# Kernel optimization log

Hardware: AMD Instinct MI355X
Metric: run time of the kernel (lower is better)

## Reference

```python
import jax, jax.numpy as jnp
import numpy as np

B, L, CH, NH, NB = 32, 512, 512, 8, 2
HD = CH // NH
NEG = -4294967295.0  # -2**32 + 1, as in the torch code


def _ln(x, g, b, eps=1e-8):
    m = x.mean(-1, keepdims=True)
    v = ((x - m) ** 2).mean(-1, keepdims=True)
    return (x - m) / jnp.sqrt(v + eps) * g + b


def _forward(log_seqs, seqs_nxt, t, qw, qb, kw, kb, vw, vb,
             ln1g, ln1b, ln2g, ln2b, c1w, c1b, c2w, c2b,
             posK, posV, lng, lnb, tw0, tb0, tw1, tb1, tw2, tb2,
             decw, decb):
    # causal mask (mode='training'): True = masked (~tril)
    mask = jnp.triu(jnp.ones((L, L), dtype=bool), k=1)
    pK = posK[:L].reshape(L, NH, HD)  # shared relative/absolute pos per head
    pV = posV[:L].reshape(L, NH, HD)
    seqs = log_seqs
    for i in range(NB):
        Qin = _ln(seqs, ln1g[i], ln1b[i])
        # note: Q from layernormed input, K/V from raw seqs (as in torch code)
        Q = (Qin @ qw[i].T + qb[i]).reshape(B, L, NH, HD)
        K = (seqs @ kw[i].T + kb[i]).reshape(B, L, NH, HD)
        V = (seqs @ vw[i].T + vb[i]).reshape(B, L, NH, HD)
        scores = jnp.einsum('blhd,bmhd->bhlm', Q, K)
        scores = scores + jnp.einsum('blhd,mhd->bhlm', Q, pK)
        scores = scores / jnp.sqrt(jnp.float32(HD))
        scores = jnp.where(mask, NEG, scores)
        w = jax.nn.softmax(scores, axis=-1)
        out = jnp.einsum('bhlm,bmhd->blhd', w, V) + jnp.einsum('bhlm,mhd->blhd', w, pV)
        seqs = Qin + out.reshape(B, L, CH)  # residual from layernormed Q
        seqs = _ln(seqs, ln2g[i], ln2b[i])
        # PointWiseFeedForward: conv1d kernel_size=1 == linear; residual inside
        h = jax.nn.relu(seqs @ c1w[i].T + c1b[i])
        seqs = seqs + (h @ c2w[i].T + c2b[i])
    log_feats = _ln(seqs, lng, lnb)

    # diffusion timestep embedding
    half = CH // 2
    freqs = jnp.exp(jnp.arange(half, dtype=jnp.float32) * (-np.log(10000.0) / (half - 1)))
    ang = t.astype(jnp.float32)[:, None] * freqs[None, :]
    temb = jnp.concatenate([jnp.sin(ang), jnp.cos(ang)], axis=1)  # [B, CH]
    temb = temb @ tw0.T + tb0
    temb = temb * jax.nn.sigmoid(temb)  # swish nonlinearity
    temb = temb @ tw1.T + tb1
    temb = temb * jax.nn.sigmoid(temb)
    temb = temb @ tw2.T + tb2
    x_t = seqs_nxt + temb[:, None, :]

    # non-conditional decoder path: decoder(cat([log_feats, x_t], -1))
    dec = jnp.concatenate([log_feats, x_t], axis=-1) @ decw.T + decb
    return (log_feats, dec)


def setup_inputs() -> dict:
    key = jax.random.key(0)
    ks = jax.random.split(key, 24)
    s = 0.02

    def n(k, shape):
        return jax.random.normal(k, shape, jnp.float32) * s

    return {
        'log_seqs': jax.random.normal(ks[0], (B, L, CH), jnp.float32),
        'seqs_nxt': jax.random.normal(ks[1], (B, L, CH), jnp.float32),
        't': jax.random.randint(ks[2], (B,), 0, 1000, jnp.int32),
        'qw': n(ks[3], (NB, CH, CH)), 'qb': jnp.zeros((NB, CH), jnp.float32),
        'kw': n(ks[4], (NB, CH, CH)), 'kb': jnp.zeros((NB, CH), jnp.float32),
        'vw': n(ks[5], (NB, CH, CH)), 'vb': jnp.zeros((NB, CH), jnp.float32),
        'ln1g': jnp.ones((NB, CH), jnp.float32), 'ln1b': jnp.zeros((NB, CH), jnp.float32),
        'ln2g': jnp.ones((NB, CH), jnp.float32), 'ln2b': jnp.zeros((NB, CH), jnp.float32),
        'c1w': n(ks[6], (NB, CH, CH)), 'c1b': jnp.zeros((NB, CH), jnp.float32),
        'c2w': n(ks[7], (NB, CH, CH)), 'c2b': jnp.zeros((NB, CH), jnp.float32),
        'posK': n(ks[8], (L, CH)), 'posV': n(ks[9], (L, CH)),
        'lng': jnp.ones((CH,), jnp.float32), 'lnb': jnp.zeros((CH,), jnp.float32),
        'tw0': n(ks[10], (4 * CH, CH)), 'tb0': jnp.zeros((4 * CH,), jnp.float32),
        'tw1': n(ks[11], (4 * CH, 4 * CH)), 'tb1': jnp.zeros((4 * CH,), jnp.float32),
        'tw2': n(ks[12], (CH, 4 * CH)), 'tb2': jnp.zeros((CH,), jnp.float32),
        'decw': n(ks[13], (CH, 2 * CH)), 'decb': jnp.zeros((CH,), jnp.float32),
    }


def reference(log_seqs, seqs_nxt, t, qw, qb, kw, kb, vw, vb,
              ln1g, ln1b, ln2g, ln2b, c1w, c1b, c2w, c2b,
              posK, posV, lng, lnb, tw0, tb0, tw1, tb1, tw2, tb2,
              decw, decb):
    return _forward(log_seqs, seqs_nxt, t, qw, qb, kw, kb, vw, vb,
                    ln1g, ln1b, ln2g, ln2b, c1w, c1b, c2w, c2b,
                    posK, posV, lng, lnb, tw0, tb0, tw1, tb1, tw2, tb2,
                    decw, decb)
```

## Files before the change

kernel.cpp:

```cpp
#include <hip/hip_runtime.h>
#include <math.h>

#define BB 32
#define LL 512
#define CHN 512
#define NHH 8
#define HDD 64

typedef __attribute__((ext_vector_type(8))) short short8;
typedef __attribute__((ext_vector_type(4))) float f32x4;

__device__ __forceinline__ float b2f(unsigned short s) {
    union { unsigned int u; float f; } c; c.u = ((unsigned int)s) << 16; return c.f;
}
__device__ __forceinline__ unsigned short f2b(float f) {
    union { float f; unsigned int u; } c; c.f = f;
    return (unsigned short)((c.u + 0x7fffu + ((c.u >> 16) & 1u)) >> 16);
}

#define SWZ(row, col) ((((row) * 64 + (col))) ^ (((row) & 7) << 3))

__device__ __forceinline__ void gl16(const unsigned short* g, unsigned short* l) {
    __builtin_amdgcn_global_load_lds(
        (const __attribute__((address_space(1))) unsigned int*)g,
        (__attribute__((address_space(3))) unsigned int*)l, 16, 0, 0);
}

__global__ __launch_bounds__(256) void cvt7_kernel(
    const float* __restrict__ p0, const float* __restrict__ p1,
    const float* __restrict__ p2, const float* __restrict__ p3,
    const float* __restrict__ p4, const float* __restrict__ p5,
    unsigned short* __restrict__ y,
    const float* __restrict__ seqs, unsigned short* __restrict__ R1)
{
    const int j = blockIdx.y;
    const int i = blockIdx.x * 256 + threadIdx.x;
    if (j < 6) {
        const float* x = j == 0 ? p0 : j == 1 ? p1 : j == 2 ? p2
                       : j == 3 ? p3 : j == 4 ? p4 : p5;
        const float4 v = reinterpret_cast<const float4*>(x)[i];
        ushort4 o;
        o.x = f2b(v.x); o.y = f2b(v.y); o.z = f2b(v.z); o.w = f2b(v.w);
        size_t dst4;
        if (j == 1)      dst4 = 131072 + i + (i >= 65536 ? 65536 : 0);
        else if (j == 2) dst4 = 131072 + 65536 + i + (i >= 65536 ? 65536 : 0);
        else             dst4 = (size_t)j * 131072 + i;
        reinterpret_cast<ushort4*>(y)[dst4] = o;
    } else {
        #pragma unroll
        for (int t = 0; t < 16; ++t) {
            const int ii = t * 131072 + i;
            const float4 v = reinterpret_cast<const float4*>(seqs)[ii];
            ushort4 o;
            o.x = f2b(v.x); o.y = f2b(v.y); o.z = f2b(v.z); o.w = f2b(v.w);
            reinterpret_cast<ushort4*>(R1)[ii] = o;
        }
    }
}

__global__ __launch_bounds__(256) void ln_kernel(
    const unsigned short* __restrict__ x, const float* __restrict__ g,
    const float* __restrict__ b, float* __restrict__ yf,
    unsigned short* __restrict__ yb)
{
    const int row = blockIdx.x;
    const int tid = threadIdx.x;
    const size_t base = (size_t)row * CHN;
    const ushort2 v2 = *reinterpret_cast<const ushort2*>(x + base + tid * 2);
    const float vx = b2f(v2.x), vy = b2f(v2.y);
    float s  = vx + vy;
    float ss = vx * vx + vy * vy;
    #pragma unroll
    for (int m = 1; m < 64; m <<= 1) {
        s  += __shfl_xor(s, m);
        ss += __shfl_xor(ss, m);
    }
    __shared__ float red[8];
    const int wave = tid >> 6;
    if ((tid & 63) == 0) { red[wave] = s; red[4 + wave] = ss; }
    __syncthreads();
    s  = red[0] + red[1] + red[2] + red[3];
    ss = red[4] + red[5] + red[6] + red[7];
    const float mean = s * (1.0f / CHN);
    const float var  = ss * (1.0f / CHN) - mean * mean;
    const float inv  = rsqrtf(var + 1e-8f);
    const int c = tid * 2;
    float ox = (vx - mean) * inv * g[c]     + b[c];
    float oy = (vy - mean) * inv * g[c + 1] + b[c + 1];
    if (yf) *reinterpret_cast<float2*>(yf + base + c) = make_float2(ox, oy);
    if (yb) {
        ushort2 ob; ob.x = f2b(ox); ob.y = f2b(oy);
        *reinterpret_cast<ushort2*>(yb + base + c) = ob;
    }
}

template <int NT, int NBX>
__device__ __forceinline__ void gemm_body(
    const unsigned short* __restrict__ A,
    const unsigned short* __restrict__ A2,
    const unsigned short* __restrict__ W, int ldw,
    const float* __restrict__ bias,
    const float* __restrict__ pos,
    const unsigned short* __restrict__ resb,
    float* __restrict__ outf,
    unsigned short* __restrict__ outb,
    unsigned short* __restrict__ outbt,
    int act, int bid,
    unsigned short* lA, unsigned short* lB)
{
    const int tid  = threadIdx.x;
    const int lane = tid & 63;
    const int wid  = tid >> 6;

    const int swz = (bid & 7) * (NBX * 8) + (bid >> 3);
    const int by = swz / NBX, bx = swz % NBX;
    const int bm = by * 256, bn = bx * 128;

    const int ia0 = wid * 2, ia1 = wid * 2 + 1;
    const int hiA0 = ia0 >> 2, rgA0 = ia0 & 3;
    const int hiA1 = ia1 >> 2, rgA1 = ia1 & 3;
    const int hiB = wid >> 1, rgB = wid & 1;

    const unsigned short* Ax = A2 ? A2 : A;
    const unsigned short* aS0  = A  + (size_t)(bm + rgA0 * 64 + lane) * 512 + hiA0 * 8;
    const unsigned short* aS1  = A  + (size_t)(bm + rgA1 * 64 + lane) * 512 + hiA1 * 8;
    const unsigned short* a2S0 = Ax + (size_t)(bm + rgA0 * 64 + lane) * 512 + hiA0 * 8;
    const unsigned short* a2S1 = Ax + (size_t)(bm + rgA1 * 64 + lane) * 512 + hiA1 * 8;
    const unsigned short* wS   = W + (size_t)(bn + rgB * 64 + lane) * ldw + hiB * 8;
    const int dA0 = (hiA0 * 256 + rgA0 * 64) * 8;
    const int dA1 = (hiA1 * 256 + rgA1 * 64) * 8;
    const int dB  = (hiB * 128 + rgB * 64) * 8;

    const int wr = wid >> 1, wc = wid & 1;
    const int fr = lane & 15;
    const int fq = lane >> 4;

    f32x4 acc[4][4];
    #pragma unroll
    for (int m = 0; m < 4; ++m)
        #pragma unroll
        for (int n = 0; n < 4; ++n)
            acc[m][n] = (f32x4){0.f, 0.f, 0.f, 0.f};

    #define MG_STAGE(buf, t)                                            \
        do {                                                            \
            const int k0 = ((t) & 15) * 32;                             \
            const unsigned short* s0 = ((t) < 16) ? aS0 : a2S0;         \
            const unsigned short* s1 = ((t) < 16) ? aS1 : a2S1;         \
            gl16(s0 + k0, &lA[(buf) * 8192 + dA0]);                     \
            gl16(s1 + k0, &lA[(buf) * 8192 + dA1]);                     \
            gl16(wS + (t) * 32, &lB[(buf) * 4096 + dB]);                \
        } while (0)

    MG_STAGE(0, 0);
    MG_STAGE(1, 1);

    #pragma unroll
    for (int t = 0; t < NT; ++t) {
        const int cur = t % 3;
        if (t + 2 < NT) {
            MG_STAGE((t + 2) % 3, t + 2);
            asm volatile("s_waitcnt vmcnt(6)" ::: "memory");
        } else if (t + 1 < NT) {
            asm volatile("s_waitcnt vmcnt(3)" ::: "memory");
        } else {
            asm volatile("s_waitcnt vmcnt(0)" ::: "memory");
        }
        __builtin_amdgcn_s_barrier();

        const unsigned short* pa = &lA[cur * 8192 + (fq * 256 + wr * 64 + fr) * 8];
        const unsigned short* pb = &lB[cur * 4096 + (fq * 128 + wc * 64 + fr) * 8];
        short8 aF[4], bF[4];
        #pragma unroll
        for (int m = 0; m < 4; ++m)
            aF[m] = *reinterpret_cast<const short8*>(pa + m * 128);
        #pragma unroll
        for (int n = 0; n < 4; ++n)
            bF[n] = *reinterpret_cast<const short8*>(pb + n * 128);
        asm volatile("s_waitcnt lgkmcnt(0)" ::: "memory");
        __builtin_amdgcn_s_barrier();

        __builtin_amdgcn_s_setprio(1);
        #pragma unroll
        for (int m = 0; m < 4; ++m)
            #pragma unroll
            for (int n = 0; n < 4; ++n)
                acc[m][n] = __builtin_amdgcn_mfma_f32_16x16x32_bf16(
                    aF[m], bF[n], acc[m][n], 0, 0, 0);
        __builtin_amdgcn_s_setprio(0);
    }
    #undef MG_STAGE

    const int row0 = bm + wr * 64, col0 = bn + wc * 64;
    #pragma unroll
    for (int m = 0; m < 4; ++m) {
        #pragma unroll
        for (int n = 0; n < 4; ++n) {
            const int col = col0 + n * 16 + fr;
            const float bia = bias ? bias[col] : 0.f;
            ushort4 o4;
            #pragma unroll
            for (int r = 0; r < 4; ++r) {
                const int row = row0 + m * 16 + fq * 4 + r;
                float v = acc[m][n][r] + bia;
                if (pos) v += pos[(size_t)(row & (LL - 1)) * CHN + col];
                if (act == 1) v = fmaxf(v, 0.f);
                else if (act == 3) v *= 0.125f;
                const size_t idx = (size_t)row * CHN + col;
                if (resb) v += b2f(resb[idx]);
                if (outf) outf[idx] = v;
                if (outb) outb[idx] = f2b(v);
                ((unsigned short*)&o4)[r] = f2b(v);
            }
            if (outbt) {
                const int rw = row0 + m * 16 + fq * 4;
                *reinterpret_cast<ushort4*>(
                    &outbt[((size_t)(rw >> 9) * 512 + col) * 512 + (rw & 511)]) = o4;
            }
        }
    }
}

__device__ __forceinline__ void kv_body(
    const unsigned short* __restrict__ A,
    const unsigned short* __restrict__ Wkv,
    const float* __restrict__ kb, const float* __restrict__ vb,
    const float* __restrict__ posK, const float* __restrict__ posV,
    unsigned short* __restrict__ KBb, unsigned short* __restrict__ VTb,
    int bid, unsigned short* lA, unsigned short* lB)
{
    const int tid  = threadIdx.x;
    const int lane = tid & 63;
    const int wid  = tid >> 6;

    const int swz = (bid & 7) * 64 + (bid >> 3);
    const int by = swz >> 3, bx = swz & 7;
    const int bm = by * 256, bn = bx * 128;

    const int ia0 = wid * 2, ia1 = wid * 2 + 1;
    const int hiA0 = ia0 >> 2, rgA0 = ia0 & 3;
    const int hiA1 = ia1 >> 2, rgA1 = ia1 & 3;
    const int hiB = wid >> 1, rgB = wid & 1;

    const unsigned short* aS0 = A + (size_t)(bm + rgA0 * 64 + lane) * 512 + hiA0 * 8;
    const unsigned short* aS1 = A + (size_t)(bm + rgA1 * 64 + lane) * 512 + hiA1 * 8;
    const unsigned short* wS  = Wkv + (size_t)(bn + rgB * 64 + lane) * 512 + hiB * 8;
    const int dA0 = (hiA0 * 256 + rgA0 * 64) * 8;
    const int dA1 = (hiA1 * 256 + rgA1 * 64) * 8;
    const int dB  = (hiB * 128 + rgB * 64) * 8;

    const int wr = wid >> 1, wc = wid & 1;
    const int fr = lane & 15;
    const int fq = lane >> 4;

    f32x4 acc[4][4];
    #pragma unroll
    for (int m = 0; m < 4; ++m)
        #pragma unroll
        for (int n = 0; n < 4; ++n)
            acc[m][n] = (f32x4){0.f, 0.f, 0.f, 0.f};

    #define KV_STAGE(buf, t)                                            \
        do {                                                            \
            const int k0 = (t) * 32;                                    \
            gl16(aS0 + k0, &lA[(buf) * 8192 + dA0]);                    \
            gl16(aS1 + k0, &lA[(buf) * 8192 + dA1]);                    \
            gl16(wS + k0, &lB[(buf) * 4096 + dB]);                      \
        } while (0)

    KV_STAGE(0, 0);
    KV_STAGE(1, 1);

    #pragma unroll
    for (int t = 0; t < 16; ++t) {
        const int cur = t % 3;
        if (t + 2 < 16) {
            KV_STAGE((t + 2) % 3, t + 2);
            asm volatile("s_waitcnt vmcnt(6)" ::: "memory");
        } else if (t + 1 < 16) {
            asm volatile("s_waitcnt vmcnt(3)" ::: "memory");
        } else {
            asm volatile("s_waitcnt vmcnt(0)" ::: "memory");
        }
        __builtin_amdgcn_s_barrier();

        const unsigned short* pa = &lA[cur * 8192 + (fq * 256 + wr * 64 + fr) * 8];
        const unsigned short* pb = &lB[cur * 4096 + (fq * 128 + wc * 64 + fr) * 8];
        short8 aF[4], bF[4];
        #pragma unroll
        for (int m = 0; m < 4; ++m)
            aF[m] = *reinterpret_cast<const short8*>(pa + m * 128);
        #pragma unroll
        for (int n = 0; n < 4; ++n)
            bF[n] = *reinterpret_cast<const short8*>(pb + n * 128);
        asm volatile("s_waitcnt lgkmcnt(0)" ::: "memory");
        __builtin_amdgcn_s_barrier();

        __builtin_amdgcn_s_setprio(1);
        #pragma unroll
        for (int m = 0; m < 4; ++m)
            #pragma unroll
            for (int n = 0; n < 4; ++n)
                acc[m][n] = __builtin_amdgcn_mfma_f32_16x16x32_bf16(
                    aF[m], bF[n], acc[m][n], 0, 0, 0);
        __builtin_amdgcn_s_setprio(0);
    }
    #undef KV_STAGE

    const int row0 = bm + wr * 64;
    if (bn < 512) {
        const int col0 = bn + wc * 64;
        #pragma unroll
        for (int m = 0; m < 4; ++m) {
            #pragma unroll
            for (int n = 0; n < 4; ++n) {
                const int col = col0 + n * 16 + fr;
                const float bia = kb[col];
                #pragma unroll
                for (int r = 0; r < 4; ++r) {
                    const int row = row0 + m * 16 + fq * 4 + r;
                    float v = acc[m][n][r] + bia
                            + posK[(size_t)(row & (LL - 1)) * CHN + col];
                    KBb[(size_t)row * CHN + col] = f2b(v);
                }
            }
        }
    } else {
        const int vcol0 = (bn - 512) + wc * 64;
        #pragma unroll
        for (int m = 0; m < 4; ++m) {
            #pragma unroll
            for (int n = 0; n < 4; ++n) {
                const int vcol = vcol0 + n * 16 + fr;
                const float bia = vb[vcol];
                ushort4 o4;
                #pragma unroll
                for (int r = 0; r < 4; ++r) {
                    const int row = row0 + m * 16 + fq * 4 + r;
                    float v = acc[m][n][r] + bia
                            + posV[(size_t)(row & (LL - 1)) * CHN + vcol];
                    ((unsigned short*)&o4)[r] = f2b(v);
                }
                const int rw = row0 + m * 16 + fq * 4;
                *reinterpret_cast<ushort4*>(
                    &VTb[((size_t)(rw >> 9) * 512 + vcol) * 512 + (rw & 511)]) = o4;
            }
        }
    }
}

__global__ __launch_bounds__(512) void mgemm_kernel(
    const unsigned short* __restrict__ A,
    const unsigned short* __restrict__ W, int ldw,
    const float* __restrict__ bias,
    const float* __restrict__ pos,
    const unsigned short* __restrict__ resb,
    float* __restrict__ outf,
    unsigned short* __restrict__ outb,
    unsigned short* __restrict__ outbt,
    int act)
{
    __shared__ alignas(16) unsigned short lA[3 * 8192];
    __shared__ alignas(16) unsigned short lB[3 * 4096];
    gemm_body<16, 4>(A, nullptr, W, ldw, bias, pos, resb, outf, outb, outbt, act,
                     blockIdx.x, lA, lB);
}

__global__ __launch_bounds__(512) void qkv2_kernel(
    const unsigned short* __restrict__ qinb, const unsigned short* __restrict__ curb,
    const unsigned short* __restrict__ Wq, const unsigned short* __restrict__ Wkv,
    const float* __restrict__ qb, const float* __restrict__ kb,
    const float* __restrict__ vb,
    const float* __restrict__ posK, const float* __restrict__ posV,
    unsigned short* __restrict__ QBb, unsigned short* __restrict__ KBb,
    unsigned short* __restrict__ VTb)
{
    __shared__ alignas(16) unsigned short lA[3 * 8192];
    __shared__ alignas(16) unsigned short lB[3 * 4096];
    if (blockIdx.x < 256) {
        gemm_body<16, 4>(qinb, nullptr, Wq, 512, qb, nullptr, nullptr,
                         nullptr, QBb, nullptr, 3, blockIdx.x, lA, lB);
    } else {
        kv_body(curb, Wkv, kb, vb, posK, posV, KBb, VTb, blockIdx.x - 256, lA, lB);
    }
}

__global__ __launch_bounds__(512) void dec_kernel(
    const unsigned short* __restrict__ R0b, const unsigned short* __restrict__ R1b,
    const unsigned short* __restrict__ Wd, const float* __restrict__ decb,
    float* __restrict__ dec)
{
    __shared__ alignas(16) unsigned short lA[3 * 8192];
    __shared__ alignas(16) unsigned short lB[3 * 4096];
    gemm_body<32, 4>(R0b, R1b, Wd, 1024, decb, nullptr, nullptr, dec, nullptr,
                     nullptr, 0, blockIdx.x, lA, lB);
}

__global__ __launch_bounds__(256) void skgemm_kernel(
    const float* __restrict__ A, int K,
    const float* __restrict__ W, int N,
    float* __restrict__ P)
{
    __shared__ float As[32][128];
    const int tid = threadIdx.x;
    const int kz  = blockIdx.y;
    const int c   = blockIdx.x * 256 + tid;

    #pragma unroll
    for (int i = 0; i < 16; ++i) {
        const int idx = i * 256 + tid;
        const int r = idx >> 7, k = idx & 127;
        As[r][k] = A[(size_t)r * K + kz * 128 + k];
    }
    __syncthreads();

    float acc[32];
    #pragma unroll
    for (int r = 0; r < 32; ++r) acc[r] = 0.f;

    const float* wrow = W + (size_t)c * K + kz * 128;
    for (int k4 = 0; k4 < 32; ++k4) {
        const float4 w = reinterpret_cast<const float4*>(wrow)[k4];
        #pragma unroll
        for (int r = 0; r < 32; ++r) {
            const float4 a = *reinterpret_cast<const float4*>(&As[r][k4 * 4]);
            acc[r] = fmaf(w.x, a.x, fmaf(w.y, a.y, fmaf(w.z, a.z, fmaf(w.w, a.w, acc[r]))));
        }
    }

    float* pp = P + ((size_t)kz * N + c) * 32;
    #pragma unroll
    for (int r = 0; r < 32; ++r) pp[r] = acc[r];
}

__global__ __launch_bounds__(256) void skreduce_kernel(
    const float* __restrict__ P, int KS, const float* __restrict__ bias,
    float* __restrict__ out, int N, int act)
{
    const int idx = blockIdx.x * 256 + threadIdx.x;
    const int r = idx & 31, c = idx >> 5;
    float s = 0.f;
    for (int kz = 0; kz < KS; ++kz)
        s += P[(size_t)kz * N * 32 + idx];
    s += bias[c];
    if (act == 2) s = s / (1.f + __expf(-s));
    out[(size_t)r * N + c] = s;
}

__global__ __launch_bounds__(256) void mattn_kernel(
    const unsigned short* __restrict__ Q, const unsigned short* __restrict__ K,
    const unsigned short* __restrict__ VT, const unsigned short* __restrict__ Qin,
    unsigned short* __restrict__ Sout)
{
    __shared__ alignas(16) unsigned short kT[2][4096];
    __shared__ alignas(16) unsigned short vT[2][4096];
    __shared__ unsigned short pl[4][1024];

    const int pr = blockIdx.x;
    const int qtA = pr, qtB = 7 - pr;
    const int h  = blockIdx.y;
    const int b  = blockIdx.z;
    const int tid = threadIdx.x, lane = tid & 63, wid = tid >> 6;
    const int fr = lane & 15, fq = lane >> 4;
    const int hc = h * HDD;

    const int c0i = tid, c1i = 256 + tid;
    const int r0s = c0i >> 3, j0s = c0i & 7, d0s = ((j0s ^ (r0s & 7)) << 3);
    const int r1s = c1i >> 3, j1s = c1i & 7, d1s = ((j1s ^ (r1s & 7)) << 3);
    const unsigned short* kS0 = K + (size_t)b * LL * CHN + (size_t)r0s * CHN + hc + d0s;
    const unsigned short* kS1 = K + (size_t)b * LL * CHN + (size_t)r1s * CHN + hc + d1s;
    const unsigned short* vS0 = VT + ((size_t)(b * NHH + h) * 64 + r0s) * 512 + d0s;
    const unsigned short* vS1 = VT + ((size_t)(b * NHH + h) * 64 + r1s) * 512 + d1s;

    #define AT_STAGE(buf, ch)                                              \
        do {                                                               \
            const int o = (ch) * 64;                                       \
            gl16(kS0 + (size_t)o * CHN, &kT[buf][wid * 512]);              \
            gl16(kS1 + (size_t)o * CHN, &kT[buf][2048 + wid * 512]);       \
            gl16(vS0 + o, &vT[buf][wid * 512]);                            \
            gl16(vS1 + o, &vT[buf][2048 + wid * 512]);                     \
        } while (0)

    const size_t qrowA = (size_t)b * LL + qtA * 64 + wid * 16 + fr;
    const size_t qrowB = (size_t)b * LL + qtB * 64 + wid * 16 + fr;
    short8 qfA[2], qfB[2];
    qfA[0] = *reinterpret_cast<const short8*>(Q + qrowA * CHN + hc + fq * 8);
    qfA[1] = *reinterpret_cast<const short8*>(Q + qrowA * CHN + hc + 32 + fq * 8);
    qfB[0] = *reinterpret_cast<const short8*>(Q + qrowB * CHN + hc + fq * 8);
    qfB[1] = *reinterpret_cast<const short8*>(Q + qrowB * CHN + hc + 32 + fq * 8);

    f32x4 oaccA[4], oaccB[4];
    float lA_[4], lB_[4];
    #pragma unroll
    for (int n = 0; n < 4; ++n) {
        oaccA[n] = (f32x4){0.f, 0.f, 0.f, 0.f};
        oaccB[n] = (f32x4){0.f, 0.f, 0.f, 0.f};
    }
    #pragma unroll
    for (int r = 0; r < 4; ++r) { lA_[r] = 0.f; lB_[r] = 0.f; }

    auto tile_step = [&](int cur, int qt, int ch, const short8* qf,
                         f32x4* oacc, float* lrow) {
        f32x4 sacc[4];
        #pragma unroll
        for (int n = 0; n < 4; ++n) sacc[n] = (f32x4){0.f, 0.f, 0.f, 0.f};
        __builtin_amdgcn_s_setprio(1);
        #pragma unroll
        for (int kk = 0; kk < 2; ++kk) {
            #pragma unroll
            for (int n = 0; n < 4; ++n) {
                const short8 kf = *reinterpret_cast<const short8*>(
                    &kT[cur][SWZ(n * 16 + fr, kk * 32 + fq * 8)]);
                sacc[n] = __builtin_amdgcn_mfma_f32_16x16x32_bf16(qf[kk], kf, sacc[n], 0, 0, 0);
            }
        }
        __builtin_amdgcn_s_setprio(0);

        const bool diag = (ch == qt);
        #pragma unroll
        for (int r = 0; r < 4; ++r) {
            float sv[4];
            #pragma unroll
            for (int n = 0; n < 4; ++n) {
                float v = sacc[n][r];
                if (diag && (n * 16 + fr > wid * 16 + fq * 4 + r)) v = -1e30f;
                sv[n] = __expf(v);
            }
            float ps = (sv[0] + sv[1]) + (sv[2] + sv[3]);
            ps += __shfl_xor(ps, 1);
            ps += __shfl_xor(ps, 2);
            ps += __shfl_xor(ps, 4);
            ps += __shfl_xor(ps, 8);
            lrow[r] += ps;
            #pragma unroll
            for (int n = 0; n < 4; ++n)
                pl[wid][SWZ(fq * 4 + r, n * 16 + fr)] = f2b(sv[n]);
        }

        __builtin_amdgcn_s_setprio(1);
        #pragma unroll
        for (int kk = 0; kk < 2; ++kk) {
            const short8 pa = *reinterpret_cast<const short8*>(
                &pl[wid][SWZ(fr, kk * 32 + fq * 8)]);
            #pragma unroll
            for (int n = 0; n < 4; ++n) {
                const short8 vf = *reinterpret_cast<const short8*>(
                    &vT[cur][SWZ(n * 16 + fr, kk * 32 + fq * 8)]);
                oacc[n] = __builtin_amdgcn_mfma_f32_16x16x32_bf16(pa, vf, oacc[n], 0, 0, 0);
            }
        }
        __builtin_amdgcn_s_setprio(0);
    };

    AT_STAGE(0, 0);
    __syncthreads();

    for (int ch = 0; ch <= qtB; ++ch) {
        const int cur = ch & 1;
        if (ch < qtB) AT_STAGE(cur ^ 1, ch + 1);

        tile_step(cur, qtB, ch, qfB, oaccB, lB_);
        if (ch <= qtA)
            tile_step(cur, qtA, ch, qfA, oaccA, lA_);

        __syncthreads();
    }
    #undef AT_STAGE

    #pragma unroll
    for (int s = 0; s < 2; ++s) {
        const int qt = s ? qtB : qtA;
        const f32x4* oacc = s ? oaccB : oaccA;
        const float* lrow = s ? lB_ : lA_;
        const size_t orow0 = (size_t)b * LL + qt * 64 + wid * 16 + fq * 4;
        #pragma unroll
        for (int r = 0; r < 4; ++r) {
            const float inv = 1.f / lrow[r];
            const size_t rowidx = (orow0 + r) * CHN + hc;
            #pragma unroll
            for (int n = 0; n < 4; ++n) {
                const int d = n * 16 + fr;
                Sout[rowidx + d] = f2b(oacc[n][r] * inv + b2f(Qin[rowidx + d]));
            }
        }
    }
}

__global__ __launch_bounds__(256) void temb_embed_kernel(
    const int* __restrict__ t, float* __restrict__ T0)
{
    const int idx = blockIdx.x * 256 + threadIdx.x;
    const int b = idx >> 9, j = idx & 511;
    const float tv = (float)t[b];
    const int jj = (j < 256) ? j : j - 256;
    const float freq = __expf((float)jj * (-9.210340371976184f / 255.f));
    const float ang = tv * freq;
    T0[idx] = (j < 256) ? sinf(ang) : cosf(ang);
}

__global__ __launch_bounds__(256) void add_temb_kernel(
    const float* __restrict__ xin, const float* __restrict__ temb,
    unsigned short* __restrict__ out)
{
    const size_t i4 = (size_t)blockIdx.x * 256 + threadIdx.x;
    const size_t elem = i4 * 4;
    const int b = (int)(elem >> 18);
    const int c = (int)(elem & (CHN - 1));
    const float4 a = reinterpret_cast<const float4*>(xin)[i4];
    const float4 tv = *reinterpret_cast<const float4*>(temb + (size_t)b * CHN + c);
    ushort4 o;
    o.x = f2b(a.x + tv.x); o.y = f2b(a.y + tv.y);
    o.z = f2b(a.z + tv.z); o.w = f2b(a.w + tv.w);
    reinterpret_cast<ushort4*>(out)[i4] = o;
}

extern "C" void kernel_launch(void* const* d_in, const int* in_sizes, int n_in,
                              void* d_out, int out_size, void* d_ws, size_t ws_size,
                              hipStream_t stream)
{
    (void)in_sizes; (void)n_in; (void)out_size; (void)ws_size;
    const float* log_seqs = (const float*)d_in[0];
    const float* seqs_nxt = (const float*)d_in[1];
    const int*   tt       = (const int*)d_in[2];
    const float* qw  = (const float*)d_in[3];
    const float* qb  = (const float*)d_in[4];
    const float* kw  = (const float*)d_in[5];
    const float* kb  = (const float*)d_in[6];
    const float* vw  = (const float*)d_in[7];
    const float* vb  = (const float*)d_in[8];
    const float* ln1g = (const float*)d_in[9];
    const float* ln1b = (const float*)d_in[10];
    const float* ln2g = (const float*)d_in[11];
    const float* ln2b = (const float*)d_in[12];
    const float* c1w = (const float*)d_in[13];
    const float* c1b = (const float*)d_in[14];
    const float* c2w = (const float*)d_in[15];
    const float* c2b = (const float*)d_in[16];
    const float* posK = (const float*)d_in[17];
    const float* posV = (const float*)d_in[18];
    const float* lng = (const float*)d_in[19];
    const float* lnb = (const float*)d_in[20];
    const float* tw0 = (const float*)d_in[21];
    const float* tb0 = (const float*)d_in[22];
    const float* tw1 = (const float*)d_in[23];
    const float* tb1 = (const float*)d_in[24];
    const float* tw2 = (const float*)d_in[25];
    const float* tb2 = (const float*)d_in[26];
    const float* decw = (const float*)d_in[27];
    const float* decb = (const float*)d_in[28];

    const size_t SZ = (size_t)BB * LL * CHN;
    const int M = BB * LL;
    float* out = (float*)d_out;
    float* log_feats = out;
    float* dec = out + SZ;
    unsigned short* QBb = (unsigned short*)dec;
    unsigned short* VTb = (unsigned short*)log_feats;

    float* ws = (float*)d_ws;
    unsigned short* SB = (unsigned short*)ws;
    float* P = ws + SZ / 2;
    unsigned short* KBb = (unsigned short*)(ws + SZ);
    unsigned short* R0  = (unsigned short*)(ws + SZ + SZ / 2);
    unsigned short* R1  = (unsigned short*)(ws + 2 * SZ);
    unsigned short* WBu = (unsigned short*)(ws + 2 * SZ + SZ / 2);
    float* T0 = ws + 2 * SZ + SZ / 2 + 1572864;
    float* T1 = T0 + 32 * CHN;
    float* T2 = T1 + 32 * 2048;
    float* T3 = T2 + 32 * 2048;

    const size_t WQ = 0, WKV = 524288, WC1 = 1572864,
                 WC2 = 2097152, WDEC = 2621440;

    auto mg = [&](const unsigned short* A, const unsigned short* W, int ldw,
                  const float* bias, const float* pos, const unsigned short* resb,
                  float* outf, unsigned short* outb, unsigned short* outbt, int act) {
        mgemm_kernel<<<256, 512, 0, stream>>>(A, W, ldw, bias, pos, resb,
                                              outf, outb, outbt, act);
    };
    auto skg = [&](const float* A, int K, const float* W, int N,
                   const float* bias, float* o, int act) {
        skgemm_kernel<<<dim3(N / 256, K / 128), 256, 0, stream>>>(A, K, W, N, P);
        skreduce_kernel<<<(N * 32) / 256, 256, 0, stream>>>(P, K / 128, bias, o, N, act);
    };

    cvt7_kernel<<<dim3(512, 7), 256, 0, stream>>>(qw, kw, vw, c1w, c2w, decw, WBu,
                                                  log_seqs, R1);

    for (int i = 0; i < 2; ++i) {
        const size_t wo = (size_t)i * 262144;
        const size_t bo = (size_t)i * CHN;

        ln_kernel<<<M, 256, 0, stream>>>(R1, ln1g + bo, ln1b + bo, nullptr, R0);
        qkv2_kernel<<<768, 512, 0, stream>>>(
            R0, R1, WBu + WQ + wo, WBu + WKV + (size_t)i * 524288,
            qb + bo, kb + bo, vb + bo, posK, posV, QBb, KBb, VTb);
        mattn_kernel<<<dim3(4, NHH, BB), 256, 0, stream>>>(QBb, KBb, VTb, R0, SB);
        ln_kernel<<<M, 256, 0, stream>>>(SB, ln2g + bo, ln2b + bo, nullptr, SB);
        mg(SB, WBu + WC1 + wo, 512, c1b + bo, nullptr, nullptr, nullptr, R0, nullptr, 1);
        mg(R0, WBu + WC2 + wo, 512, c2b + bo, nullptr, SB, nullptr, R1, nullptr, 0);
    }

    ln_kernel<<<M, 256, 0, stream>>>(R1, lng, lnb, log_feats, R0);

    temb_embed_kernel<<<(BB * CHN) / 256, 256, 0, stream>>>(tt, T0);
    skg(T0, 512, tw0, 2048, tb0, T1, 2);
    skg(T1, 2048, tw1, 2048, tb1, T2, 2);
    skg(T2, 2048, tw2, 512, tb2, T3, 0);
    add_temb_kernel<<<(M * CHN / 4) / 256, 256, 0, stream>>>(seqs_nxt, T3, R1);

    dec_kernel<<<256, 512, 0, stream>>>(R0, R1, WBu + WDEC, decb, dec);
}
```

Before: 597.4 us.

## Split paired query tiles across two wave groups in 512-thread attention blocks

The attention kernel moves from 256 to 512 threads per block. Each group of four waves now handles one of the two paired query tiles, instead of every wave processing both tiles one after the other. This roughly halves the serial per-wave work and register state (one accumulator set), which should raise parallelism and occupancy. Each thread also issues half as many staging loads. In exchange, the qtA wave group goes idle for the chunks after its diagonal tile but still waits at every barrier, and LDS use grows for the larger P buffer.

```diff
diff --git a/kernel.cpp b/kernel.cpp
--- a/kernel.cpp
+++ b/kernel.cpp
@@ -447,110 +447,48 @@
     out[(size_t)r * N + c] = s;
 }
 
-__global__ __launch_bounds__(256) void mattn_kernel(
+__global__ __launch_bounds__(512) void mattn_kernel(
     const unsigned short* __restrict__ Q, const unsigned short* __restrict__ K,
     const unsigned short* __restrict__ VT, const unsigned short* __restrict__ Qin,
     unsigned short* __restrict__ Sout)
 {
     __shared__ alignas(16) unsigned short kT[2][4096];
     __shared__ alignas(16) unsigned short vT[2][4096];
-    __shared__ unsigned short pl[4][1024];
+    __shared__ unsigned short pl[8][1024];
 
     const int pr = blockIdx.x;
     const int qtA = pr, qtB = 7 - pr;
     const int h  = blockIdx.y;
     const int b  = blockIdx.z;
     const int tid = threadIdx.x, lane = tid & 63, wid = tid >> 6;
+    const int wg = wid >> 2;
+    const int wl = wid & 3;
     const int fr = lane & 15, fq = lane >> 4;
     const int hc = h * HDD;
 
-    const int c0i = tid, c1i = 256 + tid;
-    const int r0s = c0i >> 3, j0s = c0i & 7, d0s = ((j0s ^ (r0s & 7)) << 3);
-    const int r1s = c1i >> 3, j1s = c1i & 7, d1s = ((j1s ^ (r1s & 7)) << 3);
-    const unsigned short* kS0 = K + (size_t)b * LL * CHN + (size_t)r0s * CHN + hc + d0s;
-    const unsigned short* kS1 = K + (size_t)b * LL * CHN + (size_t)r1s * CHN + hc + d1s;
-    const unsigned short* vS0 = VT + ((size_t)(b * NHH + h) * 64 + r0s) * 512 + d0s;
-    const unsigned short* vS1 = VT + ((size_t)(b * NHH + h) * 64 + r1s) * 512 + d1s;
+    const int rs = tid >> 3, js = tid & 7, ds = ((js ^ (rs & 7)) << 3);
+    const unsigned short* kS = K + (size_t)b * LL * CHN + (size_t)rs * CHN + hc + ds;
+    const unsigned short* vS = VT + ((size_t)(b * NHH + h) * 64 + rs) * 512 + ds;
 
     #define AT_STAGE(buf, ch)                                              \
         do {                                                               \
             const int o = (ch) * 64;                                       \
-            gl16(kS0 + (size_t)o * CHN, &kT[buf][wid * 512]);              \
-            gl16(kS1 + (size_t)o * CHN, &kT[buf][2048 + wid * 512]);       \
-            gl16(vS0 + o, &vT[buf][wid * 512]);                            \
-            gl16(vS1 + o, &vT[buf][2048 + wid * 512]);                     \
+            gl16(kS + (size_t)o * CHN, &kT[buf][wid * 512]);               \
+            gl16(vS + o, &vT[buf][wid * 512]);                             \
         } while (0)
 
-    const size_t qrowA = (size_t)b * LL + qtA * 64 + wid * 16 + fr;
-    const size_t qrowB = (size_t)b * LL + qtB * 64 + wid * 16 + fr;
-    short8 qfA[2], qfB[2];
-    qfA[0] = *reinterpret_cast<const short8*>(Q + qrowA * CHN + hc + fq * 8);
-    qfA[1] = *reinterpret_cast<const short8*>(Q + qrowA * CHN + hc + 32 + fq * 8);
-    qfB[0] = *reinterpret_cast<const short8*>(Q + qrowB * CHN + hc + fq * 8);
-    qfB[1] = *reinterpret_cast<const short8*>(Q + qrowB * CHN + hc + 32 + fq * 8);
-
-    f32x4 oaccA[4], oaccB[4];
-    float lA_[4], lB_[4];
-    #pragma unroll
-    for (int n = 0; n < 4; ++n) {
-        oaccA[n] = (f32x4){0.f, 0.f, 0.f, 0.f};
-        oaccB[n] = (f32x4){0.f, 0.f, 0.f, 0.f};
-    }
-    #pragma unroll
-    for (int r = 0; r < 4; ++r) { lA_[r] = 0.f; lB_[r] = 0.f; }
-
-    auto tile_step = [&](int cur, int qt, int ch, const short8* qf,
-                         f32x4* oacc, float* lrow) {
-        f32x4 sacc[4];
-        #pragma unroll
-        for (int n = 0; n < 4; ++n) sacc[n] = (f32x4){0.f, 0.f, 0.f, 0.f};
-        __builtin_amdgcn_s_setprio(1);
-        #pragma unroll
-        for (int kk = 0; kk < 2; ++kk) {
-            #pragma unroll
-            for (int n = 0; n < 4; ++n) {
-                const short8 kf = *reinterpret_cast<const short8*>(
-                    &kT[cur][SWZ(n * 16 + fr, kk * 32 + fq * 8)]);
-                sacc[n] = __builtin_amdgcn_mfma_f32_16x16x32_bf16(qf[kk], kf, sacc[n], 0, 0, 0);
-            }
-        }
-        __builtin_amdgcn_s_setprio(0);
-
-        const bool diag = (ch == qt);
-        #pragma unroll
-        for (int r = 0; r < 4; ++r) {
-            float sv[4];
-            #pragma unroll
-            for (int n = 0; n < 4; ++n) {
-                float v = sacc[n][r];
-                if (diag && (n * 16 + fr > wid * 16 + fq * 4 + r)) v = -1e30f;
-                sv[n] = __expf(v);
-            }
-            float ps = (sv[0] + sv[1]) + (sv[2] + sv[3]);
-            ps += __shfl_xor(ps, 1);
-            ps += __shfl_xor(ps, 2);
-            ps += __shfl_xor(ps, 4);
-            ps += __shfl_xor(ps, 8);
-            lrow[r] += ps;
-            #pragma unroll
-            for (int n = 0; n < 4; ++n)
-                pl[wid][SWZ(fq * 4 + r, n * 16 + fr)] = f2b(sv[n]);
-        }
-
-        __builtin_amdgcn_s_setprio(1);
-        #pragma unroll
-        for (int kk = 0; kk < 2; ++kk) {
-            const short8 pa = *reinterpret_cast<const short8*>(
-                &pl[wid][SWZ(fr, kk * 32 + fq * 8)]);
-            #pragma unroll
-            for (int n = 0; n < 4; ++n) {
-                const short8 vf = *reinterpret_cast<const short8*>(
-                    &vT[cur][SWZ(n * 16 + fr, kk * 32 + fq * 8)]);
-                oacc[n] = __builtin_amdgcn_mfma_f32_16x16x32_bf16(pa, vf, oacc[n], 0, 0, 0);
-            }
-        }
-        __builtin_amdgcn_s_setprio(0);
-    };
+    const int myQt = wg ? qtA : qtB;
+    const size_t qrow = (size_t)b * LL + myQt * 64 + wl * 16 + fr;
+    short8 qf[2];
+    qf[0] = *reinterpret_cast<const short8*>(Q + qrow * CHN + hc + fq * 8);
+    qf[1] = *reinterpret_cast<const short8*>(Q + qrow * CHN + hc + 32 + fq * 8);
+
+    f32x4 oacc[4];
+    float lrow[4];
+    #pragma unroll
+    for (int n = 0; n < 4; ++n) oacc[n] = (f32x4){0.f, 0.f, 0.f, 0.f};
+    #pragma unroll
+    for (int r = 0; r < 4; ++r) lrow[r] = 0.f;
 
     AT_STAGE(0, 0);
     __syncthreads();
@@ -559,29 +497,73 @@
         const int cur = ch & 1;
         if (ch < qtB) AT_STAGE(cur ^ 1, ch + 1);
 
-        tile_step(cur, qtB, ch, qfB, oaccB, lB_);
-        if (ch <= qtA)
-            tile_step(cur, qtA, ch, qfA, oaccA, lA_);
+        if (ch <= myQt) {
+            f32x4 sacc[4];
+            #pragma unroll
+            for (int n = 0; n < 4; ++n) sacc[n] = (f32x4){0.f, 0.f, 0.f, 0.f};
+            __builtin_amdgcn_s_setprio(1);
+            #pragma unroll
+            for (int kk = 0; kk < 2; ++kk) {
+                #pragma unroll
+                for (int n = 0; n < 4; ++n) {
+                    const short8 kf = *reinterpret_cast<const short8*>(
+                        &kT[cur][SWZ(n * 16 + fr, kk * 32 + fq * 8)]);
+                    sacc[n] = __builtin_amdgcn_mfma_f32_16x16x32_bf16(
+                        qf[kk], kf, sacc[n], 0, 0, 0);
+                }
+            }
+            __builtin_amdgcn_s_setprio(0);
+
+            const bool diag = (ch == myQt);
+            #pragma unroll
+            for (int r = 0; r < 4; ++r) {
+                float sv[4];
+                #pragma unroll
+                for (int n = 0; n < 4; ++n) {
+                    float v = sacc[n][r];
+                    if (diag && (n * 16 + fr > wl * 16 + fq * 4 + r)) v = -1e30f;
+                    sv[n] = __expf(v);
+                }
+                float ps = (sv[0] + sv[1]) + (sv[2] + sv[3]);
+                ps += __shfl_xor(ps, 1);
+                ps += __shfl_xor(ps, 2);
+                ps += __shfl_xor(ps, 4);
+                ps += __shfl_xor(ps, 8);
+                lrow[r] += ps;
+                #pragma unroll
+                for (int n = 0; n < 4; ++n)
+                    pl[wid][SWZ(fq * 4 + r, n * 16 + fr)] = f2b(sv[n]);
+            }
+
+            __builtin_amdgcn_s_setprio(1);
+            #pragma unroll
+            for (int kk = 0; kk < 2; ++kk) {
+                const short8 pa = *reinterpret_cast<const short8*>(
+                    &pl[wid][SWZ(fr, kk * 32 + fq * 8)]);
+                #pragma unroll
+                for (int n = 0; n < 4; ++n) {
+                    const short8 vf = *reinterpret_cast<const short8*>(
+                        &vT[cur][SWZ(n * 16 + fr, kk * 32 + fq * 8)]);
+                    oacc[n] = __builtin_amdgcn_mfma_f32_16x16x32_bf16(
+                        pa, vf, oacc[n], 0, 0, 0);
+                }
+            }
+            __builtin_amdgcn_s_setprio(0);
+        }
 
         __syncthreads();
     }
     #undef AT_STAGE
 
-    #pragma unroll
-    for (int s = 0; s < 2; ++s) {
-        const int qt = s ? qtB : qtA;
-        const f32x4* oacc = s ? oaccB : oaccA;
-        const float* lrow = s ? lB_ : lA_;
-        const size_t orow0 = (size_t)b * LL + qt * 64 + wid * 16 + fq * 4;
-        #pragma unroll
-        for (int r = 0; r < 4; ++r) {
-            const float inv = 1.f / lrow[r];
-            const size_t rowidx = (orow0 + r) * CHN + hc;
-            #pragma unroll
-            for (int n = 0; n < 4; ++n) {
-                const int d = n * 16 + fr;
-                Sout[rowidx + d] = f2b(oacc[n][r] * inv + b2f(Qin[rowidx + d]));
-            }
+    const size_t orow0 = (size_t)b * LL + myQt * 64 + wl * 16 + fq * 4;
+    #pragma unroll
+    for (int r = 0; r < 4; ++r) {
+        const float inv = 1.f / lrow[r];
+        const size_t rowidx = (orow0 + r) * CHN + hc;
+        #pragma unroll
+        for (int n = 0; n < 4; ++n) {
+            const int d = n * 16 + fr;
+            Sout[rowidx + d] = f2b(oacc[n][r] * inv + b2f(Qin[rowidx + d]));
         }
     }
 }
@@ -695,7 +677,7 @@
         qkv2_kernel<<<768, 512, 0, stream>>>(
             R0, R1, WBu + WQ + wo, WBu + WKV + (size_t)i * 524288,
             qb + bo, kb + bo, vb + bo, posK, posV, QBb, KBb, VTb);
-        mattn_kernel<<<dim3(4, NHH, BB), 256, 0, stream>>>(QBb, KBb, VTb, R0, SB);
+        mattn_kernel<<<dim3(4, NHH, BB), 512, 0, stream>>>(QBb, KBb, VTb, R0, SB);
         ln_kernel<<<M, 256, 0, stream>>>(SB, ln2g + bo, ln2b + bo, nullptr, SB);
         mg(SB, WBu + WC1 + wo, 512, c1b + bo, nullptr, nullptr, nullptr, R0, nullptr, 1);
         mg(R0, WBu + WC2 + wo, 512, c2b + bo, nullptr, SB, nullptr, R1, nullptr, 0);
```

After: 591.3 us. About the same (-1.0%).
